# Optimization experiments

Measured on AMD Instinct MI355X. Metric: run time of the kernel, lower is better.

The kernel has to match this reference:

```python
import jax, jax.numpy as jnp
import numpy as np
import itertools

N_BOX = 19
B = 2048
T = 5
_EDGES = np.array(list(itertools.combinations(range(N_BOX), 2)))  # [E,2], E=171
ROW = jnp.asarray(_EDGES[:, 0])
COL = jnp.asarray(_EDGES[:, 1])


def setup_inputs() -> dict:
    key = jax.random.key(0)
    ks = jax.random.split(key, 8)
    return {
        "location_t": jax.random.uniform(ks[0], (B, N_BOX, 5), dtype=jnp.float32),
        "feature_t": jax.random.normal(ks[1], (B, N_BOX, 512), dtype=jnp.float32),
        "mask_t": jax.random.randint(ks[2], (B, N_BOX), 0, 2).astype(bool),
        "past_location_t": jax.random.uniform(ks[3], (B, T, N_BOX, 6), dtype=jnp.float32),
        "W1": jax.random.normal(ks[4], (512, 256), dtype=jnp.float32) * 0.05,
        "b1": jax.random.normal(ks[5], (256,), dtype=jnp.float32) * 0.05,
        "W2": jax.random.normal(ks[6], (256, 512), dtype=jnp.float32) * 0.05,
        "b2": jax.random.normal(ks[7], (512,), dtype=jnp.float32) * 0.05,
    }


def _edge_weights(location_t, mask, past_location_t):
    # bbox centers from cols 1..4: [B,N]
    cx = 0.5 * (location_t[:, :, 1] + location_t[:, :, 3])
    cy = 0.5 * (location_t[:, :, 2] + location_t[:, :, 4])
    d = (cx[:, ROW] - cx[:, COL]) ** 2 + (cy[:, ROW] - cy[:, COL]) ** 2  # [B,E]

    # motion distance, vectorized over all nodes then gathered per edge
    cp = past_location_t[:, :, :, 3:-1] - past_location_t[:, :, :, 1:3]  # [B,T,N,2]
    cpx = cp[..., 0] * 1280.0  # [B,T,N]
    cpy = cp[..., 1] * 720.0
    dx = cpx[:, -1] - cpx[:, 0]  # [B,N]
    dy = cpy[:, -1] - cpy[:, 0]
    length = jnp.sqrt(dx ** 2 + dy ** 2)
    length = jnp.where(length == 0.0, 1.0, length)
    ndx = dx / length
    ndy = dy / length
    x0 = cpx[:, 0]  # [B,N]
    y0 = cpy[:, 0]
    d1 = jnp.sqrt((x0[:, ROW] + ndx[:, ROW] - x0[:, COL] - ndx[:, COL]) ** 2
                  + (y0[:, ROW] + ndy[:, ROW] - y0[:, COL] - ndy[:, COL]) ** 2)
    d2 = jnp.sqrt((x0[:, ROW] - x0[:, COL]) ** 2 + (y0[:, ROW] - y0[:, COL]) ** 2)
    md = d1 - d2  # [B,E]

    w = jnp.exp(-(0.7 * d + 0.3 * md))
    valid = mask[:, ROW] & mask[:, COL]
    w = jnp.where(valid, w, 0.0)
    wmin = jnp.min(w, axis=1, keepdims=True)
    wmax = jnp.max(w, axis=1, keepdims=True)
    return (w - wmin) / (wmax - wmin)


def _gcn(x, ew, W, b):
    # PyG GCNConv: add self loops (weight 1), symmetric normalization, x@W, scatter-add, +bias
    n = x.shape[0]
    loops = jnp.arange(n)
    row = jnp.concatenate([ROW, loops])
    col = jnp.concatenate([COL, loops])
    ew_full = jnp.concatenate([ew, jnp.ones((n,), ew.dtype)])
    deg = jax.ops.segment_sum(ew_full, col, num_segments=n)
    dinv = jnp.where(deg > 0, deg ** -0.5, 0.0)
    norm = dinv[row] * ew_full * dinv[col]  # [E+N]
    xw = x @ W  # [N,F_out]
    out = jnp.zeros((n, W.shape[1]), xw.dtype).at[col].add(norm[:, None] * xw[row])
    return out + b


def reference(location_t, feature_t, mask_t, past_location_t, W1, b1, W2, b2):
    w = _edge_weights(location_t, mask_t, past_location_t)  # [B,E]

    def per_graph(x, ew):
        h = jax.nn.sigmoid(_gcn(x, ew, W1, b1))
        return jax.nn.sigmoid(_gcn(h, ew, W2, b2))

    return jax.vmap(per_graph)(feature_t, w)  # [B,19,512]
```

## Files before the change

kernel.cpp:

```cpp
#include <hip/hip_runtime.h>
#include <hip/hip_bf16.h>
#include <math.h>

#define NBOX 19
#define NEDGE 171
#define TT 5
#define BATCH 2048
#define GB 2
#define MR (GB * NBOX)
#define MP 48

typedef __attribute__((ext_vector_type(8))) short short8v;
typedef __attribute__((ext_vector_type(4))) float f32x4;

static __device__ __forceinline__ ushort f2bf(float f) {
    __hip_bfloat16 h = __float2bfloat16(f);
    return *reinterpret_cast<ushort*>(&h);
}

__device__ __forceinline__ int edge_index(int r, int c) {
    return r * (NBOX - 1) - (r * (r - 1)) / 2 + (c - r - 1);
}

__global__ __launch_bounds__(192) void adjbf_kernel(
    const float* __restrict__ loc,
    const int*   __restrict__ mask,
    const float* __restrict__ past,
    ushort* __restrict__ adjbf)
{
    int b = blockIdx.x;
    int tid = threadIdx.x;
    __shared__ float cx[NBOX], cy[NBOX], x0[NBOX], y0[NBOX], ndx[NBOX], ndy[NBOX];
    __shared__ int   mv[NBOX];
    __shared__ float w[NEDGE];
    __shared__ float dinv[NBOX];
    __shared__ float wmin_s, wmax_s;

    if (tid < NBOX) {
        const float* l = loc + ((size_t)b * NBOX + tid) * 5;
        cx[tid] = 0.5f * (l[1] + l[3]);
        cy[tid] = 0.5f * (l[2] + l[4]);
        const float* p0 = past + (((size_t)b * TT + 0) * NBOX + tid) * 6;
        const float* p4 = past + (((size_t)b * TT + (TT - 1)) * NBOX + tid) * 6;
        float cpx0 = (p0[3] - p0[1]) * 1280.0f, cpy0 = (p0[4] - p0[2]) * 720.0f;
        float cpx4 = (p4[3] - p4[1]) * 1280.0f, cpy4 = (p4[4] - p4[2]) * 720.0f;
        float dx = cpx4 - cpx0, dy = cpy4 - cpy0;
        float len = sqrtf(dx * dx + dy * dy);
        if (len == 0.0f) len = 1.0f;
        ndx[tid] = dx / len;
        ndy[tid] = dy / len;
        x0[tid] = cpx0;
        y0[tid] = cpy0;
        mv[tid] = mask[(size_t)b * NBOX + tid];
    }
    __syncthreads();

    float wv = 0.0f;
    if (tid < NEDGE) {
        int rem = tid, rr = 0;
        while (rem >= NBOX - 1 - rr) { rem -= NBOX - 1 - rr; rr++; }
        int r = rr, c = rr + 1 + rem;
        float ddx = cx[r] - cx[c], ddy = cy[r] - cy[c];
        float d = ddx * ddx + ddy * ddy;
        float ax = x0[r] + ndx[r] - x0[c] - ndx[c];
        float ay = y0[r] + ndy[r] - y0[c] - ndy[c];
        float d1 = sqrtf(ax * ax + ay * ay);
        float bx = x0[r] - x0[c], by = y0[r] - y0[c];
        float d2 = sqrtf(bx * bx + by * by);
        float md = d1 - d2;
        wv = expf(-(0.7f * d + 0.3f * md));
        if (!(mv[r] && mv[c])) wv = 0.0f;
        w[tid] = wv;
    }
    __syncthreads();

    if (tid == 0) {
        float mn = w[0], mx = w[0];
        for (int i = 1; i < NEDGE; i++) { mn = fminf(mn, w[i]); mx = fmaxf(mx, w[i]); }
        wmin_s = mn; wmax_s = mx;
    }
    __syncthreads();

    float inv_range = 1.0f / (wmax_s - wmin_s);
    if (tid < NEDGE) w[tid] = (wv - wmin_s) * inv_range;
    __syncthreads();

    if (tid < NBOX) {
        float s = 1.0f;
        for (int rr = 0; rr < tid; rr++) s += w[edge_index(rr, tid)];
        dinv[tid] = 1.0f / sqrtf(s);
    }
    __syncthreads();

    ushort* A = adjbf + (size_t)b * 1024;
    for (int idx = tid; idx < 1024; idx += 192) {
        int r = idx & 31, cc = idx >> 5;
        float v = 0.0f;
        if (r < NBOX && cc < NBOX) {
            if (r == cc) v = dinv[r] * dinv[r];
            else if (r < cc) v = w[edge_index(r, cc)] * dinv[r] * dinv[cc];
        }
        A[idx] = f2bf(v);
    }
}

__global__ void packT_kernel(const float* __restrict__ src, ushort* __restrict__ dst,
                             int K, int N)
{
    int total = K * N;
    for (int idx = blockIdx.x * blockDim.x + threadIdx.x; idx < total;
         idx += gridDim.x * blockDim.x) {
        int n = idx / K, k = idx % K;
        dst[idx] = f2bf(src[(size_t)k * N + n]);
    }
}

__global__ __launch_bounds__(256, 4) void fused_kernel(
    const float*  __restrict__ feat,
    const ushort* __restrict__ adjbf,
    const ushort* __restrict__ W1T,
    const ushort* __restrict__ W2T,
    const float*  __restrict__ b1,
    const float*  __restrict__ b2,
    float* __restrict__ out)
{
    __shared__ __align__(16) ushort XHs[MP * 256];
    __shared__ __align__(16) ushort YsT[64 * 64];
    __shared__ __align__(16) ushort AdjS[MP * 64];

    const int tid = threadIdx.x;
    const int lane = tid & 63, wv = tid >> 6;
    const int rowbase = blockIdx.x * MR;
    const int bbase = blockIdx.x * GB;
    const int ncol = wv * 16 + (lane & 15);
    const int kgrp = lane >> 4;
    const int l15 = lane & 15;

#pragma unroll
    for (int p = 0; p < 2; p++)
        ((int4*)YsT)[tid + p * 256] = make_int4(0, 0, 0, 0);

    for (int i = tid; i < MP * 64; i += 256) {
        int row = i >> 6, col = i & 63;
        ushort v = 0;
        if (row < MR) {
            int g = (row >= NBOX) ? 1 : 0;
            int cc = row - g * NBOX;
            int rc = col - g * NBOX;
            if ((unsigned)rc < (unsigned)NBOX)
                v = adjbf[(size_t)(bbase + g) * 1024 + cc * 32 + rc];
        }
        int boff = (row * 128 + col * 2) ^ ((row & 7) << 4);
        *(ushort*)((char*)AdjS + boff) = v;
    }

    f32x4 acc1[4][3];
#pragma unroll
    for (int c = 0; c < 4; c++)
#pragma unroll
        for (int m = 0; m < 3; m++) acc1[c][m] = (f32x4){0.f, 0.f, 0.f, 0.f};

    for (int kh = 0; kh < 2; kh++) {
        __syncthreads();
        const float* fg = feat + (size_t)rowbase * 512 + kh * 256;
#pragma unroll
        for (int p = 0; p < 12; p++) {
            int i = tid + p * 256;
            int row = i >> 6, q = i & 63;
            ushort4 h;
            if (i < MR * 64) {
                float4 v = *(const float4*)(fg + (size_t)row * 512 + q * 4);
                h.x = f2bf(v.x); h.y = f2bf(v.y); h.z = f2bf(v.z); h.w = f2bf(v.w);
            } else {
                h.x = 0; h.y = 0; h.z = 0; h.w = 0;
            }
            int boff = (row * 512 + q * 8) ^ ((row & 7) << 4);
            *(ushort4*)((char*)XHs + boff) = h;
        }
        __syncthreads();

        const ushort* bpb = W1T + (size_t)ncol * 512 + kh * 256 + kgrp * 8;
        short8v bcur[4], bnxt[4];
#pragma unroll
        for (int c = 0; c < 4; c++)
            bcur[c] = *(const short8v*)(bpb + (size_t)c * 64 * 512);
#pragma unroll
        for (int ks = 0; ks < 8; ks++) {
            if (ks < 7) {
#pragma unroll
                for (int c = 0; c < 4; c++)
                    bnxt[c] = *(const short8v*)(bpb + (size_t)c * 64 * 512 + (ks + 1) * 32);
            }
            short8v a[3];
#pragma unroll
            for (int m = 0; m < 3; m++) {
                int row = m * 16 + l15;
                int boff = (row * 512 + ks * 64 + kgrp * 16) ^ ((row & 7) << 4);
                a[m] = *(const short8v*)((char*)XHs + boff);
            }
#pragma unroll
            for (int c = 0; c < 4; c++)
#pragma unroll
                for (int m = 0; m < 3; m++)
                    acc1[c][m] = __builtin_amdgcn_mfma_f32_16x16x32_bf16(
                        a[m], bcur[c], acc1[c][m], 0, 0, 0);
#pragma unroll
            for (int c = 0; c < 4; c++) bcur[c] = bnxt[c];
        }
    }

#pragma unroll
    for (int c = 0; c < 4; c++) {
        __syncthreads();
#pragma unroll
        for (int m = 0; m < 3; m++) {
            int gr0 = m * 16 + kgrp * 4;
            ushort4 hq;
            hq.x = f2bf(acc1[c][m][0]); hq.y = f2bf(acc1[c][m][1]);
            hq.z = f2bf(acc1[c][m][2]); hq.w = f2bf(acc1[c][m][3]);
            int boff = (ncol * 128 + gr0 * 2) ^ ((ncol & 7) << 4);
            *(ushort4*)((char*)YsT + boff) = hq;
        }
        __syncthreads();
        short8v yb[2];
#pragma unroll
        for (int ks = 0; ks < 2; ks++)
            yb[ks] = *(const short8v*)((char*)YsT +
                     ((ncol * 128 + ks * 64 + kgrp * 16) ^ ((ncol & 7) << 4)));
        float bv = b1[c * 64 + ncol];
#pragma unroll
        for (int mt = 0; mt < 3; mt++) {
            f32x4 o = (f32x4){0.f, 0.f, 0.f, 0.f};
#pragma unroll
            for (int ks = 0; ks < 2; ks++) {
                int ar = mt * 16 + l15;
                short8v af = *(const short8v*)((char*)AdjS +
                             ((ar * 128 + ks * 64 + kgrp * 16) ^ ((ar & 7) << 4)));
                o = __builtin_amdgcn_mfma_f32_16x16x32_bf16(af, yb[ks], o, 0, 0, 0);
            }
#pragma unroll
            for (int j = 0; j < 4; j++) {
                int grp = mt * 16 + kgrp * 4 + j;
                float s = 1.0f / (1.0f + expf(-(o[j] + bv)));
                int boff = (grp * 512 + (c * 64 + ncol) * 2) ^ ((grp & 7) << 4);
                *(ushort*)((char*)XHs + boff) = f2bf(s);
            }
        }
    }
    __syncthreads();

#pragma unroll 1
    for (int half = 0; half < 2; half++) {
        f32x4 acc[4][3];
#pragma unroll
        for (int c = 0; c < 4; c++)
#pragma unroll
            for (int m = 0; m < 3; m++) acc[c][m] = (f32x4){0.f, 0.f, 0.f, 0.f};

        const ushort* bpb = W2T + (size_t)(half * 256 + ncol) * 256 + kgrp * 8;
        short8v bcur[4], bnxt[4];
#pragma unroll
        for (int c = 0; c < 4; c++)
            bcur[c] = *(const short8v*)(bpb + (size_t)c * 64 * 256);
#pragma unroll
        for (int ks = 0; ks < 8; ks++) {
            if (ks < 7) {
#pragma unroll
                for (int c = 0; c < 4; c++)
                    bnxt[c] = *(const short8v*)(bpb + (size_t)c * 64 * 256 + (ks + 1) * 32);
            }
            short8v a[3];
#pragma unroll
            for (int m = 0; m < 3; m++) {
                int row = m * 16 + l15;
                int boff = (row * 512 + ks * 64 + kgrp * 16) ^ ((row & 7) << 4);
                a[m] = *(const short8v*)((char*)XHs + boff);
            }
#pragma unroll
            for (int c = 0; c < 4; c++)
#pragma unroll
                for (int m = 0; m < 3; m++)
                    acc[c][m] = __builtin_amdgcn_mfma_f32_16x16x32_bf16(
                        a[m], bcur[c], acc[c][m], 0, 0, 0);
#pragma unroll
            for (int c = 0; c < 4; c++) bcur[c] = bnxt[c];
        }

#pragma unroll
        for (int c = 0; c < 4; c++) {
            int cg = half * 4 + c;
            __syncthreads();
#pragma unroll
            for (int m = 0; m < 3; m++) {
                int gr0 = m * 16 + kgrp * 4;
                ushort4 hq;
                hq.x = f2bf(acc[c][m][0]); hq.y = f2bf(acc[c][m][1]);
                hq.z = f2bf(acc[c][m][2]); hq.w = f2bf(acc[c][m][3]);
                int boff = (ncol * 128 + gr0 * 2) ^ ((ncol & 7) << 4);
                *(ushort4*)((char*)YsT + boff) = hq;
            }
            __syncthreads();
            short8v yb[2];
#pragma unroll
            for (int ks = 0; ks < 2; ks++)
                yb[ks] = *(const short8v*)((char*)YsT +
                         ((ncol * 128 + ks * 64 + kgrp * 16) ^ ((ncol & 7) << 4)));
            float bv = b2[cg * 64 + ncol];
#pragma unroll
            for (int mt = 0; mt < 3; mt++) {
                f32x4 o = (f32x4){0.f, 0.f, 0.f, 0.f};
#pragma unroll
                for (int ks = 0; ks < 2; ks++) {
                    int ar = mt * 16 + l15;
                    short8v af = *(const short8v*)((char*)AdjS +
                                 ((ar * 128 + ks * 64 + kgrp * 16) ^ ((ar & 7) << 4)));
                    o = __builtin_amdgcn_mfma_f32_16x16x32_bf16(af, yb[ks], o, 0, 0, 0);
                }
#pragma unroll
                for (int j = 0; j < 4; j++) {
                    int grp = mt * 16 + kgrp * 4 + j;
                    if (grp < MR) {
                        float s = 1.0f / (1.0f + expf(-(o[j] + bv)));
                        out[(size_t)(rowbase + grp) * 512 + cg * 64 + ncol] = s;
                    }
                }
            }
        }
    }
}

extern "C" void kernel_launch(void* const* d_in, const int* in_sizes, int n_in,
                              void* d_out, int out_size, void* d_ws, size_t ws_size,
                              hipStream_t stream) {
    const float* loc  = (const float*)d_in[0];
    const float* feat = (const float*)d_in[1];
    const int*   mask = (const int*)d_in[2];
    const float* past = (const float*)d_in[3];
    const float* W1   = (const float*)d_in[4];
    const float* b1   = (const float*)d_in[5];
    const float* W2   = (const float*)d_in[6];
    const float* b2   = (const float*)d_in[7];

    ushort* adjbf = (ushort*)d_ws;
    ushort* W1T   = adjbf + (size_t)BATCH * 1024;
    ushort* W2T   = W1T + 256 * 512;

    adjbf_kernel<<<BATCH, 192, 0, stream>>>(loc, mask, past, adjbf);
    packT_kernel<<<512, 256, 0, stream>>>(W1, W1T, 512, 256);
    packT_kernel<<<256, 256, 0, stream>>>(W2, W2T, 256, 512);

    fused_kernel<<<BATCH / GB, 256, 0, stream>>>(feat, adjbf, W1T, W2T, b1, b2,
                                                 (float*)d_out);
}
```

Measured before the change: 120.9 us.

## Process one graph per block, pre-convert features to bf16, use fast sigmoid

```diff
diff --git a/kernel.cpp b/kernel.cpp
--- a/kernel.cpp
+++ b/kernel.cpp
@@ -6,9 +6,7 @@
 #define NEDGE 171
 #define TT 5
 #define BATCH 2048
-#define GB 2
-#define MR (GB * NBOX)
-#define MP 48
+#define MP 32
 
 typedef __attribute__((ext_vector_type(8))) short short8v;
 typedef __attribute__((ext_vector_type(4))) float f32x4;
@@ -16,6 +14,10 @@
 static __device__ __forceinline__ ushort f2bf(float f) {
     __hip_bfloat16 h = __float2bfloat16(f);
     return *reinterpret_cast<ushort*>(&h);
+}
+
+static __device__ __forceinline__ float sigm(float x) {
+    return __builtin_amdgcn_rcpf(1.0f + __expf(-x));
 }
 
 __device__ __forceinline__ int edge_index(int r, int c) {
@@ -115,8 +117,22 @@
     }
 }
 
-__global__ __launch_bounds__(256, 4) void fused_kernel(
-    const float*  __restrict__ feat,
+__global__ __launch_bounds__(256) void cvt_kernel(
+    const float* __restrict__ src, ushort* __restrict__ dst, int n8)
+{
+    for (int i = blockIdx.x * blockDim.x + threadIdx.x; i < n8;
+         i += gridDim.x * blockDim.x) {
+        float4 a = ((const float4*)src)[2 * i];
+        float4 b = ((const float4*)src)[2 * i + 1];
+        ushort u[8];
+        u[0] = f2bf(a.x); u[1] = f2bf(a.y); u[2] = f2bf(a.z); u[3] = f2bf(a.w);
+        u[4] = f2bf(b.x); u[5] = f2bf(b.y); u[6] = f2bf(b.z); u[7] = f2bf(b.w);
+        *(int4*)(dst + (size_t)i * 8) = *(int4*)u;
+    }
+}
+
+__global__ __launch_bounds__(256, 6) void fused_kernel(
+    const ushort* __restrict__ Xbf,
     const ushort* __restrict__ adjbf,
     const ushort* __restrict__ W1T,
     const ushort* __restrict__ W2T,
@@ -125,75 +141,54 @@
     float* __restrict__ out)
 {
     __shared__ __align__(16) ushort XHs[MP * 256];
-    __shared__ __align__(16) ushort YsT[64 * 64];
+    __shared__ __align__(16) ushort YsT[64 * 32];
     __shared__ __align__(16) ushort AdjS[MP * 64];
 
     const int tid = threadIdx.x;
-    const int lane = tid & 63, wv = tid >> 6;
-    const int rowbase = blockIdx.x * MR;
-    const int bbase = blockIdx.x * GB;
-    const int ncol = wv * 16 + (lane & 15);
+    const int lane = tid & 63, wvi = tid >> 6;
+    const int b = blockIdx.x;
+    const int ncol = wvi * 16 + (lane & 15);
     const int kgrp = lane >> 4;
     const int l15 = lane & 15;
 
-#pragma unroll
-    for (int p = 0; p < 2; p++)
-        ((int4*)YsT)[tid + p * 256] = make_int4(0, 0, 0, 0);
-
-    for (int i = tid; i < MP * 64; i += 256) {
-        int row = i >> 6, col = i & 63;
-        ushort v = 0;
-        if (row < MR) {
-            int g = (row >= NBOX) ? 1 : 0;
-            int cc = row - g * NBOX;
-            int rc = col - g * NBOX;
-            if ((unsigned)rc < (unsigned)NBOX)
-                v = adjbf[(size_t)(bbase + g) * 1024 + cc * 32 + rc];
-        }
-        int boff = (row * 128 + col * 2) ^ ((row & 7) << 4);
-        *(ushort*)((char*)AdjS + boff) = v;
-    }
-
-    f32x4 acc1[4][3];
+    {
+        int row = tid >> 3, g = tid & 7;
+        int4 v = make_int4(0, 0, 0, 0);
+        if (g < 4) v = *(const int4*)(adjbf + (size_t)b * 1024 + row * 32 + g * 8);
+        int boff = (row * 128 + g * 16) ^ ((row & 7) << 4);
+        *(int4*)((char*)AdjS + boff) = v;
+    }
+
+    f32x4 acc1[4][2];
 #pragma unroll
     for (int c = 0; c < 4; c++)
 #pragma unroll
-        for (int m = 0; m < 3; m++) acc1[c][m] = (f32x4){0.f, 0.f, 0.f, 0.f};
-
+        for (int m = 0; m < 2; m++) acc1[c][m] = (f32x4){0.f, 0.f, 0.f, 0.f};
+
+    const ushort* xg = Xbf + (size_t)b * NBOX * 512;
     for (int kh = 0; kh < 2; kh++) {
         __syncthreads();
-        const float* fg = feat + (size_t)rowbase * 512 + kh * 256;
-#pragma unroll
-        for (int p = 0; p < 12; p++) {
+#pragma unroll
+        for (int p = 0; p < 4; p++) {
             int i = tid + p * 256;
-            int row = i >> 6, q = i & 63;
-            ushort4 h;
-            if (i < MR * 64) {
-                float4 v = *(const float4*)(fg + (size_t)row * 512 + q * 4);
-                h.x = f2bf(v.x); h.y = f2bf(v.y); h.z = f2bf(v.z); h.w = f2bf(v.w);
-            } else {
-                h.x = 0; h.y = 0; h.z = 0; h.w = 0;
-            }
-            int boff = (row * 512 + q * 8) ^ ((row & 7) << 4);
-            *(ushort4*)((char*)XHs + boff) = h;
+            int row = i >> 5, g = i & 31;
+            int4 v = make_int4(0, 0, 0, 0);
+            if (row < NBOX) v = *(const int4*)(xg + (size_t)row * 512 + kh * 256 + g * 8);
+            int boff = (row * 512 + g * 16) ^ ((row & 7) << 4);
+            *(int4*)((char*)XHs + boff) = v;
         }
         __syncthreads();
 
         const ushort* bpb = W1T + (size_t)ncol * 512 + kh * 256 + kgrp * 8;
-        short8v bcur[4], bnxt[4];
-#pragma unroll
-        for (int c = 0; c < 4; c++)
-            bcur[c] = *(const short8v*)(bpb + (size_t)c * 64 * 512);
 #pragma unroll
         for (int ks = 0; ks < 8; ks++) {
-            if (ks < 7) {
-#pragma unroll
-                for (int c = 0; c < 4; c++)
-                    bnxt[c] = *(const short8v*)(bpb + (size_t)c * 64 * 512 + (ks + 1) * 32);
-            }
-            short8v a[3];
-#pragma unroll
-            for (int m = 0; m < 3; m++) {
+            short8v bb[4];
+#pragma unroll
+            for (int c = 0; c < 4; c++)
+                bb[c] = *(const short8v*)(bpb + (size_t)c * 64 * 512 + ks * 32);
+            short8v a[2];
+#pragma unroll
+            for (int m = 0; m < 2; m++) {
                 int row = m * 16 + l15;
                 int boff = (row * 512 + ks * 64 + kgrp * 16) ^ ((row & 7) << 4);
                 a[m] = *(const short8v*)((char*)XHs + boff);
@@ -201,11 +196,9 @@
 #pragma unroll
             for (int c = 0; c < 4; c++)
 #pragma unroll
-                for (int m = 0; m < 3; m++)
+                for (int m = 0; m < 2; m++)
                     acc1[c][m] = __builtin_amdgcn_mfma_f32_16x16x32_bf16(
-                        a[m], bcur[c], acc1[c][m], 0, 0, 0);
-#pragma unroll
-            for (int c = 0; c < 4; c++) bcur[c] = bnxt[c];
+                        a[m], bb[c], acc1[c][m], 0, 0, 0);
         }
     }
 
@@ -213,35 +206,29 @@
     for (int c = 0; c < 4; c++) {
         __syncthreads();
 #pragma unroll
-        for (int m = 0; m < 3; m++) {
+        for (int m = 0; m < 2; m++) {
             int gr0 = m * 16 + kgrp * 4;
             ushort4 hq;
             hq.x = f2bf(acc1[c][m][0]); hq.y = f2bf(acc1[c][m][1]);
             hq.z = f2bf(acc1[c][m][2]); hq.w = f2bf(acc1[c][m][3]);
-            int boff = (ncol * 128 + gr0 * 2) ^ ((ncol & 7) << 4);
+            int boff = (ncol * 64 + gr0 * 2) ^ ((ncol & 3) << 4);
             *(ushort4*)((char*)YsT + boff) = hq;
         }
         __syncthreads();
-        short8v yb[2];
-#pragma unroll
-        for (int ks = 0; ks < 2; ks++)
-            yb[ks] = *(const short8v*)((char*)YsT +
-                     ((ncol * 128 + ks * 64 + kgrp * 16) ^ ((ncol & 7) << 4)));
+        short8v yb = *(const short8v*)((char*)YsT +
+                     ((ncol * 64 + kgrp * 16) ^ ((ncol & 3) << 4)));
         float bv = b1[c * 64 + ncol];
 #pragma unroll
-        for (int mt = 0; mt < 3; mt++) {
-            f32x4 o = (f32x4){0.f, 0.f, 0.f, 0.f};
-#pragma unroll
-            for (int ks = 0; ks < 2; ks++) {
-                int ar = mt * 16 + l15;
-                short8v af = *(const short8v*)((char*)AdjS +
-                             ((ar * 128 + ks * 64 + kgrp * 16) ^ ((ar & 7) << 4)));
-                o = __builtin_amdgcn_mfma_f32_16x16x32_bf16(af, yb[ks], o, 0, 0, 0);
-            }
+        for (int mt = 0; mt < 2; mt++) {
+            int ar = mt * 16 + l15;
+            short8v af = *(const short8v*)((char*)AdjS +
+                         ((ar * 128 + kgrp * 16) ^ ((ar & 7) << 4)));
+            f32x4 o = __builtin_amdgcn_mfma_f32_16x16x32_bf16(
+                af, yb, (f32x4){0.f, 0.f, 0.f, 0.f}, 0, 0, 0);
 #pragma unroll
             for (int j = 0; j < 4; j++) {
                 int grp = mt * 16 + kgrp * 4 + j;
-                float s = 1.0f / (1.0f + expf(-(o[j] + bv)));
+                float s = sigm(o[j] + bv);
                 int boff = (grp * 512 + (c * 64 + ncol) * 2) ^ ((grp & 7) << 4);
                 *(ushort*)((char*)XHs + boff) = f2bf(s);
             }
@@ -251,27 +238,22 @@
 
 #pragma unroll 1
     for (int half = 0; half < 2; half++) {
-        f32x4 acc[4][3];
+        f32x4 acc[4][2];
 #pragma unroll
         for (int c = 0; c < 4; c++)
 #pragma unroll
-            for (int m = 0; m < 3; m++) acc[c][m] = (f32x4){0.f, 0.f, 0.f, 0.f};
+            for (int m = 0; m < 2; m++) acc[c][m] = (f32x4){0.f, 0.f, 0.f, 0.f};
 
         const ushort* bpb = W2T + (size_t)(half * 256 + ncol) * 256 + kgrp * 8;
-        short8v bcur[4], bnxt[4];
-#pragma unroll
-        for (int c = 0; c < 4; c++)
-            bcur[c] = *(const short8v*)(bpb + (size_t)c * 64 * 256);
 #pragma unroll
         for (int ks = 0; ks < 8; ks++) {
-            if (ks < 7) {
-#pragma unroll
-                for (int c = 0; c < 4; c++)
-                    bnxt[c] = *(const short8v*)(bpb + (size_t)c * 64 * 256 + (ks + 1) * 32);
-            }
-            short8v a[3];
-#pragma unroll
-            for (int m = 0; m < 3; m++) {
+            short8v bb[4];
+#pragma unroll
+            for (int c = 0; c < 4; c++)
+                bb[c] = *(const short8v*)(bpb + (size_t)c * 64 * 256 + ks * 32);
+            short8v a[2];
+#pragma unroll
+            for (int m = 0; m < 2; m++) {
                 int row = m * 16 + l15;
                 int boff = (row * 512 + ks * 64 + kgrp * 16) ^ ((row & 7) << 4);
                 a[m] = *(const short8v*)((char*)XHs + boff);
@@ -279,11 +261,9 @@
 #pragma unroll
             for (int c = 0; c < 4; c++)
 #pragma unroll
-                for (int m = 0; m < 3; m++)
+                for (int m = 0; m < 2; m++)
                     acc[c][m] = __builtin_amdgcn_mfma_f32_16x16x32_bf16(
-                        a[m], bcur[c], acc[c][m], 0, 0, 0);
-#pragma unroll
-            for (int c = 0; c < 4; c++) bcur[c] = bnxt[c];
+                        a[m], bb[c], acc[c][m], 0, 0, 0);
         }
 
 #pragma unroll
@@ -291,37 +271,31 @@
             int cg = half * 4 + c;
             __syncthreads();
 #pragma unroll
-            for (int m = 0; m < 3; m++) {
+            for (int m = 0; m < 2; m++) {
                 int gr0 = m * 16 + kgrp * 4;
                 ushort4 hq;
                 hq.x = f2bf(acc[c][m][0]); hq.y = f2bf(acc[c][m][1]);
                 hq.z = f2bf(acc[c][m][2]); hq.w = f2bf(acc[c][m][3]);
-                int boff = (ncol * 128 + gr0 * 2) ^ ((ncol & 7) << 4);
+                int boff = (ncol * 64 + gr0 * 2) ^ ((ncol & 3) << 4);
                 *(ushort4*)((char*)YsT + boff) = hq;
             }
             __syncthreads();
-            short8v yb[2];
-#pragma unroll
-            for (int ks = 0; ks < 2; ks++)
-                yb[ks] = *(const short8v*)((char*)YsT +
-                         ((ncol * 128 + ks * 64 + kgrp * 16) ^ ((ncol & 7) << 4)));
+            short8v yb = *(const short8v*)((char*)YsT +
+                         ((ncol * 64 + kgrp * 16) ^ ((ncol & 3) << 4)));
             float bv = b2[cg * 64 + ncol];
 #pragma unroll
-            for (int mt = 0; mt < 3; mt++) {
-                f32x4 o = (f32x4){0.f, 0.f, 0.f, 0.f};
-#pragma unroll
-                for (int ks = 0; ks < 2; ks++) {
-                    int ar = mt * 16 + l15;
-                    short8v af = *(const short8v*)((char*)AdjS +
-                                 ((ar * 128 + ks * 64 + kgrp * 16) ^ ((ar & 7) << 4)));
-                    o = __builtin_amdgcn_mfma_f32_16x16x32_bf16(af, yb[ks], o, 0, 0, 0);
-                }
+            for (int mt = 0; mt < 2; mt++) {
+                int ar = mt * 16 + l15;
+                short8v af = *(const short8v*)((char*)AdjS +
+                             ((ar * 128 + kgrp * 16) ^ ((ar & 7) << 4)));
+                f32x4 o = __builtin_amdgcn_mfma_f32_16x16x32_bf16(
+                    af, yb, (f32x4){0.f, 0.f, 0.f, 0.f}, 0, 0, 0);
 #pragma unroll
                 for (int j = 0; j < 4; j++) {
                     int grp = mt * 16 + kgrp * 4 + j;
-                    if (grp < MR) {
-                        float s = 1.0f / (1.0f + expf(-(o[j] + bv)));
-                        out[(size_t)(rowbase + grp) * 512 + cg * 64 + ncol] = s;
+                    if (grp < NBOX) {
+                        float s = sigm(o[j] + bv);
+                        out[((size_t)b * NBOX + grp) * 512 + cg * 64 + ncol] = s;
                     }
                 }
             }
@@ -344,11 +318,13 @@
     ushort* adjbf = (ushort*)d_ws;
     ushort* W1T   = adjbf + (size_t)BATCH * 1024;
     ushort* W2T   = W1T + 256 * 512;
+    ushort* Xbf   = W2T + 512 * 256;
 
     adjbf_kernel<<<BATCH, 192, 0, stream>>>(loc, mask, past, adjbf);
     packT_kernel<<<512, 256, 0, stream>>>(W1, W1T, 512, 256);
     packT_kernel<<<256, 256, 0, stream>>>(W2, W2T, 256, 512);
-
-    fused_kernel<<<BATCH / GB, 256, 0, stream>>>(feat, adjbf, W1T, W2T, b1, b2,
-                                                 (float*)d_out);
-}
+    cvt_kernel<<<2048, 256, 0, stream>>>(feat, Xbf, BATCH * NBOX * 512 / 8);
+
+    fused_kernel<<<BATCH, 256, 0, stream>>>(Xbf, adjbf, W1T, W2T, b1, b2,
+                                            (float*)d_out);
+}
```

New measurement: 203.1 us. +67.9%, slower.
